# Kernel optimization log

Measured on AMD Instinct MI355X. Metric: run time of the kernel, lower is better.

The kernel has to match this reference:

```python
import jax, jax.numpy as jnp
import numpy as np

B, T, I, H, O = 64, 512, 512, 1024, 512


def setup_inputs() -> dict:
    key = jax.random.key(0)
    ks = jax.random.split(key, 11)
    s_gate = 1.0 / np.sqrt(I + H)
    s_fc = 1.0 / np.sqrt(H)
    return {
        "x": jax.random.normal(ks[0], (B, T, I), dtype=jnp.float32),
        "W_f": jax.random.uniform(ks[1], (H, I + H), jnp.float32, -s_gate, s_gate),
        "b_f": jax.random.uniform(ks[2], (H,), jnp.float32, -s_gate, s_gate),
        "W_i": jax.random.uniform(ks[3], (H, I + H), jnp.float32, -s_gate, s_gate),
        "b_i": jax.random.uniform(ks[4], (H,), jnp.float32, -s_gate, s_gate),
        "W_c": jax.random.uniform(ks[5], (H, I + H), jnp.float32, -s_gate, s_gate),
        "b_c": jax.random.uniform(ks[6], (H,), jnp.float32, -s_gate, s_gate),
        "W_o": jax.random.uniform(ks[7], (H, I + H), jnp.float32, -s_gate, s_gate),
        "b_o": jax.random.uniform(ks[8], (H,), jnp.float32, -s_gate, s_gate),
        "W_fc": jax.random.uniform(ks[9], (O, H), jnp.float32, -s_fc, s_fc),
        "b_fc": jax.random.uniform(ks[10], (O,), jnp.float32, -s_fc, s_fc),
    }


def reference(x, W_f, b_f, W_i, b_i, W_c, b_c, W_o, b_o, W_fc, b_fc):
    batch = x.shape[0]
    hidden = W_f.shape[0]
    # Concatenate the 4 gate weights into one GEMM per step (same math).
    W_all = jnp.concatenate([W_f, W_i, W_c, W_o], axis=0)   # [4H, I+H]
    b_all = jnp.concatenate([b_f, b_i, b_c, b_o], axis=0)   # [4H]

    def step(carry, x_t):
        h, c = carry
        combined = jnp.concatenate([x_t, h], axis=1)         # [B, I+H]
        gates = combined @ W_all.T + b_all                   # [B, 4H]
        f_t = jax.nn.sigmoid(gates[:, :hidden])
        i_t = jax.nn.sigmoid(gates[:, hidden:2 * hidden])
        c_tilde = jnp.tanh(gates[:, 2 * hidden:3 * hidden])
        o_t = jax.nn.sigmoid(gates[:, 3 * hidden:])
        c_new = f_t * c + i_t * c_tilde
        h_new = o_t * jnp.tanh(c_new)
        y = h_new @ W_fc.T + b_fc                            # [B, O]
        return (h_new, c_new), y

    h0 = jnp.zeros((batch, hidden), x.dtype)
    c0 = jnp.zeros((batch, hidden), x.dtype)
    (h, c), ys = jax.lax.scan(step, (h0, c0), jnp.swapaxes(x, 0, 1))
    return jnp.swapaxes(ys, 0, 1), (h, c)
```

## Files before the change

kernel.cpp:

```cpp
#include <hip/hip_runtime.h>
#include <stdint.h>

#define BB 64
#define TT 512
#define II 512
#define HH 1024
#define OO 512
#define NBLK 256
#define NTHR 512
#define NB 16
#define US 16

#define WS_HBUF  1280
#define WS_ASLAB 66816
#define WS_YSLAB 3212544
#define BTO (BB*TT*OO)
#define BH  (BB*HH)

#define L_HB_U4 1024
#define L_YP_F  12288
#define L_XP_F  (12288 + 1280)
#define L_BYTES ((13568 + 1024) * 4)

typedef __fp16 v8hf __attribute__((ext_vector_type(8)));
typedef float f32x4 __attribute__((ext_vector_type(4)));
typedef _Float16 h2 __attribute__((ext_vector_type(2)));

static __device__ __forceinline__ v8hf bc8(uint4 v) { return __builtin_bit_cast(v8hf, v); }
static __device__ __forceinline__ uint32_t pk_u32(float a, float b) {
  return __builtin_bit_cast(uint32_t, __builtin_amdgcn_cvt_pkrtz(a, b));
}

__device__ __forceinline__ float sigm(float v) { return 1.0f / (1.0f + __expf(-v)); }
__device__ __forceinline__ float tanh_c(float v) {
  v = fminf(fmaxf(v, -20.0f), 20.0f);
  float e = __expf(-2.0f * v);
  return (1.0f - e) / (1.0f + e);
}

__device__ __forceinline__ uint2 cohere_ld8(const void* p) {
  unsigned long long q = __hip_atomic_load((const unsigned long long*)p,
                                           __ATOMIC_RELAXED, __HIP_MEMORY_SCOPE_AGENT);
  return __builtin_bit_cast(uint2, q);
}
__device__ __forceinline__ void cohere_st8(void* p, uint32_t lo, uint32_t hi) {
  uint2 v = make_uint2(lo, hi);
  __hip_atomic_store((unsigned long long*)p, __builtin_bit_cast(unsigned long long, v),
                     __ATOMIC_RELAXED, __HIP_MEMORY_SCOPE_AGENT);
}
__device__ __forceinline__ void cohere_st4(void* p, uint32_t v) {
  __hip_atomic_store((uint32_t*)p, v, __ATOMIC_RELAXED, __HIP_MEMORY_SCOPE_AGENT);
}

__global__ void __launch_bounds__(256) prep(
    const float* __restrict__ Wf, const float* __restrict__ Wi,
    const float* __restrict__ Wc, const float* __restrict__ Wo,
    const float* __restrict__ Wfc, float* __restrict__ ws)
{
  const int NA = 64 * 4 * 48 * 64;
  const int NY = 64 * 32 * 64;
  int idx = blockIdx.x * 256 + threadIdx.x;
  if (idx < NA) {
    int s = idx / (4 * 48 * 64);
    int rem = idx % (4 * 48 * 64);
    int mt = rem / (48 * 64);
    int rem2 = rem % (48 * 64);
    int ks = rem2 >> 6, ln = rem2 & 63;
    int r = ln & 15, kq = ln >> 4;
    int unit = s * 16 + mt * 4 + (r >> 2), gate = r & 3;
    const float* W = (gate == 0) ? Wf : (gate == 1) ? Wi : (gate == 2) ? Wc : Wo;
    const float* src = W + (size_t)unit * 1536 + ks * 32 + kq * 8;
    uint32_t p[4];
    #pragma unroll
    for (int j = 0; j < 4; ++j) {
      h2 t; t.x = (_Float16)src[2*j]; t.y = (_Float16)src[2*j+1];
      p[j] = __builtin_bit_cast(uint32_t, t);
    }
    ((uint4*)(ws + WS_ASLAB))[idx] = make_uint4(p[0], p[1], p[2], p[3]);
  } else if (idx < NA + NY) {
    int j2 = idx - NA;
    int s = j2 / (32 * 64);
    int rem = j2 % (32 * 64);
    int ks = rem >> 6, ln = rem & 63;
    int r = ln & 15, kq = ln >> 4;
    uint4 outv = make_uint4(0, 0, 0, 0);
    if (r < 8) {
      const float* src = Wfc + (size_t)(s * 8 + r) * 1024 + ks * 32 + kq * 8;
      uint32_t p[4];
      #pragma unroll
      for (int j = 0; j < 4; ++j) {
        h2 t; t.x = (_Float16)src[2*j]; t.y = (_Float16)src[2*j+1];
        p[j] = __builtin_bit_cast(uint32_t, t);
      }
      outv = make_uint4(p[0], p[1], p[2], p[3]);
    }
    ((uint4*)(ws + WS_YSLAB))[j2] = outv;
  }
}

__global__ void __launch_bounds__(NTHR, 2)
lstm_kernel(const float* __restrict__ x,
            const float* __restrict__ bf, const float* __restrict__ bi,
            const float* __restrict__ bc, const float* __restrict__ bo,
            const float* __restrict__ bfc,
            float* __restrict__ out, float* __restrict__ ws)
{
  extern __shared__ float ldsf[];
  uint4* acts4 = (uint4*)ldsf;
  float* ypart = ldsf + L_YP_F;
  float* xpart = ldsf + L_XP_F;

  const int tid  = threadIdx.x;
  const int blk  = blockIdx.x;
  const int wave = tid >> 6;
  const int lane = tid & 63;
  const bool isGate = (wave < 4);
  const int mt = wave & 3;
  const int g = blk >> 6, s = blk & 63;
  const int b0 = g * NB;
  const int u0 = s * US;

  uint32_t* ctrl  = (uint32_t*)ws;
  uint32_t* flags = ctrl + g * 128;
  ushort* hb16 = (ushort*)(ws + WS_HBUF);

  const int bq = lane & 15, kq = lane >> 4;
  const int tid2 = tid & 255;
  const int sb = tid2 >> 4, sj = tid2 & 15;
  const int gb = tid >> 5, gj = tid & 31;

  v8hf Ah[32];
  v8hf Ax[16];
  v8hf Yw[8];
  if (isGate) {
    const uint4* wpA = (const uint4*)(ws + WS_ASLAB)
                     + ((size_t)(s * 4 + mt) * 48 + 16) * 64 + lane;
    #pragma unroll
    for (int k = 0; k < 32; ++k) Ah[k] = bc8(wpA[k * 64]);
  } else {
    const uint4* wpA = (const uint4*)(ws + WS_ASLAB)
                     + ((size_t)(s * 4 + mt) * 48) * 64 + lane;
    #pragma unroll
    for (int k = 0; k < 16; ++k) Ax[k] = bc8(wpA[k * 64]);
    const uint4* wpY = (const uint4*)(ws + WS_YSLAB)
                     + ((size_t)(s * 32 + mt * 8)) * 64 + lane;
    #pragma unroll
    for (int k = 0; k < 8; ++k) Yw[k] = bc8(wpY[k * 64]);
  }
  const int unit = u0 + mt * 4 + kq;
  const float bsf = isGate ? bf[unit] : 0.f;
  const float bsi = isGate ? bi[unit] : 0.f;
  const float bsc = isGate ? bc[unit] : 0.f;
  const float bso = isGate ? bo[unit] : 0.f;
  const float ybias = (tid < 128) ? bfc[s * 8 + (tid >> 4)] : 0.0f;
  float cstate = 0.0f;

  if (!isGate) {
    const float* xs = x + ((size_t)(b0 + sb) * TT + 0) * II + sj * 32;
    #pragma unroll
    for (int v = 0; v < 4; ++v) {
      float4 u = ((const float4*)xs)[2*v], w = ((const float4*)xs)[2*v+1];
      acts4[sj * 64 + v * 16 + (sb ^ (sj & 7))] =
          make_uint4(pk_u32(u.x,u.y), pk_u32(u.z,u.w), pk_u32(w.x,w.y), pk_u32(w.z,w.w));
    }
  } else {
    #pragma unroll
    for (int j = 0; j < 8; ++j)
      acts4[L_HB_U4 + tid2 * 8 + j] = make_uint4(0,0,0,0);
  }
  __syncthreads();
  if (!isGate) {
    f32x4 ac[4];
    #pragma unroll
    for (int j = 0; j < 4; ++j) ac[j] = (f32x4){0.f,0.f,0.f,0.f};
    #pragma unroll
    for (int ks = 0; ks < 16; ++ks) {
      uint4 bv = acts4[ks * 64 + kq * 16 + (bq ^ (ks & 7))];
      ac[ks & 3] = __builtin_amdgcn_mfma_f32_16x16x32_f16(Ax[ks], bc8(bv), ac[ks & 3], 0, 0, 0);
    }
    f32x4 t = (ac[0] + ac[1]) + (ac[2] + ac[3]);
    float* xp = xpart + (mt * 64 + lane) * 4;
    xp[0] = t[0]; xp[1] = t[1]; xp[2] = t[2]; xp[3] = t[3];
  }
  __syncthreads();

  for (int it = 0; it <= TT; ++it) {
    const bool xok = (it + 1 < TT);

    if (isGate) {
      if (it < TT) {
        const float* xp = xpart + (mt * 64 + lane) * 4;
        f32x4 ac[4];
        ac[0] = (f32x4){xp[0], xp[1], xp[2], xp[3]};
        ac[1] = (f32x4){0.f,0.f,0.f,0.f};
        ac[2] = (f32x4){0.f,0.f,0.f,0.f};
        ac[3] = (f32x4){0.f,0.f,0.f,0.f};
        #pragma unroll
        for (int ksh = 0; ksh < 32; ++ksh) {
          uint4 bv = acts4[L_HB_U4 + ksh * 64 + kq * 16 + (bq ^ (ksh & 7))];
          ac[ksh & 3] = __builtin_amdgcn_mfma_f32_16x16x32_f16(Ah[ksh], bc8(bv), ac[ksh & 3], 0, 0, 0);
        }
        f32x4 t = (ac[0] + ac[1]) + (ac[2] + ac[3]);

        float gf = sigm(t[0] + bsf);
        float gi = sigm(t[1] + bsi);
        float gc = tanh_c(t[2] + bsc);
        float go = sigm(t[3] + bso);
        cstate = gf * cstate + gi * gc;
        float hv = go * tanh_c(cstate);

        uint32_t hu = (uint32_t)__builtin_bit_cast(unsigned short, (_Float16)hv);
        uint32_t pA  = hu | ((uint32_t)__shfl_down((int)hu, 16) << 16);
        uint32_t hiw = (uint32_t)__shfl_down((int)pA, 32);
        if (kq == 0) {
          ushort* hp = hb16 + (size_t)((it + 1) & 1) * BH
                     + (size_t)(b0 + bq) * HH + (u0 + mt * 4);
          cohere_st8(hp, pA, hiw);
        }
        if (it == TT - 1) {
          out[(size_t)BTO + (size_t)(b0 + bq) * HH + unit] = hv;
          out[(size_t)BTO + BH + (size_t)(b0 + bq) * HH + unit] = cstate;
        }
        asm volatile("s_waitcnt vmcnt(0)" ::: "memory");
      }
    } else {
      if (it > 0) {
        f32x4 yc = (f32x4){0.f,0.f,0.f,0.f};
        #pragma unroll
        for (int k = 0; k < 8; ++k) {
          int ksh = mt * 8 + k;
          uint4 bv = acts4[L_HB_U4 + ksh * 64 + kq * 16 + (bq ^ (ksh & 7))];
          yc = __builtin_amdgcn_mfma_f32_16x16x32_f16(Yw[k], bc8(bv), yc, 0, 0, 0);
        }
        float* yp = ypart + (mt * 64 + lane) * 5;
        yp[0] = yc[0]; yp[1] = yc[1]; yp[2] = yc[2]; yp[3] = yc[3];
      }
    }
    __syncthreads();

    if (it < TT && tid == 0)
      cohere_st4(&flags[s], (uint32_t)(it + 1));

    if (tid < 128 && it > 0) {
      int fb = tid & 15, rr = tid >> 4;
      int l = (rr >> 2) * 16 + fb;
      float yv = ybias;
      #pragma unroll
      for (int w = 0; w < 4; ++w) yv += ypart[(w * 64 + l) * 5 + (rr & 3)];
      out[(size_t)(b0 + fb) * (TT * OO) + (size_t)(it - 1) * OO + s * 8 + rr] = yv;
    }
    if (!isGate && xok) {
      const float* xs = x + ((size_t)(b0 + sb) * TT + (it + 1)) * II + sj * 32;
      float4 xr[8];
      #pragma unroll
      for (int v = 0; v < 8; ++v) xr[v] = ((const float4*)xs)[v];
      #pragma unroll
      for (int v = 0; v < 4; ++v)
        acts4[sj * 64 + v * 16 + (sb ^ (sj & 7))] =
            make_uint4(pk_u32(xr[2*v].x, xr[2*v].y), pk_u32(xr[2*v].z, xr[2*v].w),
                       pk_u32(xr[2*v+1].x, xr[2*v+1].y), pk_u32(xr[2*v+1].z, xr[2*v+1].w));
    }
    __syncthreads();

    if (!isGate && xok) {
      f32x4 ac[4];
      #pragma unroll
      for (int j = 0; j < 4; ++j) ac[j] = (f32x4){0.f,0.f,0.f,0.f};
      #pragma unroll
      for (int ks = 0; ks < 16; ++ks) {
        uint4 bv = acts4[ks * 64 + kq * 16 + (bq ^ (ks & 7))];
        ac[ks & 3] = __builtin_amdgcn_mfma_f32_16x16x32_f16(Ax[ks], bc8(bv), ac[ks & 3], 0, 0, 0);
      }
      f32x4 t = (ac[0] + ac[1]) + (ac[2] + ac[3]);
      float* xp = xpart + (mt * 64 + lane) * 4;
      xp[0] = t[0]; xp[1] = t[1]; xp[2] = t[2]; xp[3] = t[3];
    }

    if (it < TT) {
      {
        const uint32_t tgt = (uint32_t)(it + 1);
        for (;;) {
          uint2 f = cohere_ld8(&flags[gj * 2]);
          if (f.x >= tgt && f.y >= tgt) break;
          __builtin_amdgcn_s_sleep(1);
        }
        const ushort* hs = hb16 + (size_t)((it + 1) & 1) * BH
                         + (size_t)(b0 + gb) * HH + gj * 32;
        uint2 q[8];
        #pragma unroll
        for (int m = 0; m < 8; ++m) q[m] = cohere_ld8(hs + m * 4);
        #pragma unroll
        for (int sub = 0; sub < 4; ++sub)
          acts4[L_HB_U4 + gj * 64 + sub * 16 + (gb ^ (gj & 7))] =
              make_uint4(q[2*sub].x, q[2*sub].y, q[2*sub+1].x, q[2*sub+1].y);
      }
      __syncthreads();
    }
  }
}

extern "C" void kernel_launch(void* const* d_in, const int* in_sizes, int n_in,
                              void* d_out, int out_size, void* d_ws, size_t ws_size,
                              hipStream_t stream) {
  (void)in_sizes; (void)n_in; (void)out_size; (void)ws_size;
  const float* x   = (const float*)d_in[0];
  const float* Wf  = (const float*)d_in[1];
  const float* bf  = (const float*)d_in[2];
  const float* Wi  = (const float*)d_in[3];
  const float* bi  = (const float*)d_in[4];
  const float* Wc  = (const float*)d_in[5];
  const float* bc  = (const float*)d_in[6];
  const float* Wo  = (const float*)d_in[7];
  const float* bo  = (const float*)d_in[8];
  const float* Wfc = (const float*)d_in[9];
  const float* bfc = (const float*)d_in[10];
  float* out = (float*)d_out;
  float* ws  = (float*)d_ws;

  (void)hipMemsetAsync(d_ws, 0, (size_t)WS_HBUF * sizeof(float), stream);

  const int nprep = 64 * 4 * 48 * 64 + 64 * 32 * 64;
  prep<<<dim3((nprep + 255) / 256), dim3(256), 0, stream>>>(Wf, Wi, Wc, Wo, Wfc, ws);

  lstm_kernel<<<dim3(NBLK), dim3(NTHR), L_BYTES, stream>>>(
      x, bf, bi, bc, bo, bfc, out, ws);
}
```

Measured before the change: 3.331 ms.

## Replace flag-based step sync with step-tagged hidden-state packets

Result: slower. 6.171 ms (+85.2%).

```diff
diff --git a/kernel.cpp b/kernel.cpp
--- a/kernel.cpp
+++ b/kernel.cpp
@@ -11,9 +11,9 @@
 #define NB 16
 #define US 16
 
-#define WS_HBUF  1280
-#define WS_ASLAB 66816
-#define WS_YSLAB 3212544
+#define WS_HPK   1280
+#define WS_ASLAB 132352
+#define WS_YSLAB (132352 + 3145728)
 #define BTO (BB*TT*OO)
 #define BH  (BB*HH)
 
@@ -47,9 +47,6 @@
   uint2 v = make_uint2(lo, hi);
   __hip_atomic_store((unsigned long long*)p, __builtin_bit_cast(unsigned long long, v),
                      __ATOMIC_RELAXED, __HIP_MEMORY_SCOPE_AGENT);
-}
-__device__ __forceinline__ void cohere_st4(void* p, uint32_t v) {
-  __hip_atomic_store((uint32_t*)p, v, __ATOMIC_RELAXED, __HIP_MEMORY_SCOPE_AGENT);
 }
 
 __global__ void __launch_bounds__(256) prep(
@@ -120,10 +117,7 @@
   const int b0 = g * NB;
   const int u0 = s * US;
 
-  uint32_t* ctrl  = (uint32_t*)ws;
-  uint32_t* flags = ctrl + g * 128;
-  ushort* hb16 = (ushort*)(ws + WS_HBUF);
-
+  uint2* hpk = (uint2*)(ws + WS_HPK);
   const int bq = lane & 15, kq = lane >> 4;
   const int tid2 = tid & 255;
   const int sb = tid2 >> 4, sj = tid2 & 15;
@@ -210,18 +204,16 @@
         float hv = go * tanh_c(cstate);
 
         uint32_t hu = (uint32_t)__builtin_bit_cast(unsigned short, (_Float16)hv);
-        uint32_t pA  = hu | ((uint32_t)__shfl_down((int)hu, 16) << 16);
-        uint32_t hiw = (uint32_t)__shfl_down((int)pA, 32);
-        if (kq == 0) {
-          ushort* hp = hb16 + (size_t)((it + 1) & 1) * BH
-                     + (size_t)(b0 + bq) * HH + (u0 + mt * 4);
-          cohere_st8(hp, pA, hiw);
+        uint32_t pair = hu | ((uint32_t)__shfl_down((int)hu, 16) << 16);
+        if ((kq & 1) == 0) {
+          size_t pidx = (size_t)((it + 1) & 1) * (BB * 512)
+                      + (size_t)(b0 + bq) * 512 + (s * 8 + mt * 2 + (kq >> 1));
+          cohere_st8(&hpk[pidx], pair, (uint32_t)(it + 1));
         }
         if (it == TT - 1) {
           out[(size_t)BTO + (size_t)(b0 + bq) * HH + unit] = hv;
           out[(size_t)BTO + BH + (size_t)(b0 + bq) * HH + unit] = cstate;
         }
-        asm volatile("s_waitcnt vmcnt(0)" ::: "memory");
       }
     } else {
       if (it > 0) {
@@ -238,9 +230,6 @@
     }
     __syncthreads();
 
-    if (it < TT && tid == 0)
-      cohere_st4(&flags[s], (uint32_t)(it + 1));
-
     if (tid < 128 && it > 0) {
       int fb = tid & 15, rr = tid >> 4;
       int l = (rr >> 2) * 16 + fb;
@@ -277,23 +266,30 @@
     }
 
     if (it < TT) {
+      uint32_t w[16];
       {
         const uint32_t tgt = (uint32_t)(it + 1);
+        const uint2* src = hpk + (size_t)((it + 1) & 1) * (BB * 512)
+                         + (size_t)(b0 + gb) * 512 + gj * 16;
         for (;;) {
-          uint2 f = cohere_ld8(&flags[gj * 2]);
-          if (f.x >= tgt && f.y >= tgt) break;
+          uint2 p[16];
+          #pragma unroll
+          for (int m = 0; m < 16; ++m) p[m] = cohere_ld8(&src[m]);
+          uint32_t bad = 0;
+          #pragma unroll
+          for (int m = 0; m < 16; ++m) bad |= (p[m].y ^ tgt);
+          if (bad == 0) {
+            #pragma unroll
+            for (int m = 0; m < 16; ++m) w[m] = p[m].x;
+            break;
+          }
           __builtin_amdgcn_s_sleep(1);
         }
-        const ushort* hs = hb16 + (size_t)((it + 1) & 1) * BH
-                         + (size_t)(b0 + gb) * HH + gj * 32;
-        uint2 q[8];
-        #pragma unroll
-        for (int m = 0; m < 8; ++m) q[m] = cohere_ld8(hs + m * 4);
-        #pragma unroll
-        for (int sub = 0; sub < 4; ++sub)
-          acts4[L_HB_U4 + gj * 64 + sub * 16 + (gb ^ (gj & 7))] =
-              make_uint4(q[2*sub].x, q[2*sub].y, q[2*sub+1].x, q[2*sub+1].y);
-      }
+      }
+      #pragma unroll
+      for (int sub = 0; sub < 4; ++sub)
+        acts4[L_HB_U4 + gj * 64 + sub * 16 + (gb ^ (gj & 7))] =
+            make_uint4(w[4*sub], w[4*sub+1], w[4*sub+2], w[4*sub+3]);
       __syncthreads();
     }
   }
@@ -317,7 +313,6 @@
   float* out = (float*)d_out;
   float* ws  = (float*)d_ws;
 
-  (void)hipMemsetAsync(d_ws, 0, (size_t)WS_HBUF * sizeof(float), stream);
 
   const int nprep = 64 * 4 * 48 * 64 + 64 * 32 * 64;
   prep<<<dim3((nprep + 255) / 256), dim3(256), 0, stream>>>(Wf, Wi, Wc, Wo, Wfc, ws);
```
